# Kernel tuning notes

Hardware: AMD Instinct MI355X
Metric: run time of the kernel (lower is better)

The kernel has to match this reference:

```python
import jax, jax.numpy as jnp
import numpy as np

B, L, D = 4096, 200, 64


def setup_inputs() -> dict:
    key = jax.random.key(0)
    ks = jax.random.split(key, 7)
    target_key = jax.random.normal(ks[0], (B, D), dtype=jnp.float32)
    item_keys = jax.random.normal(ks[1], (B, L, D), dtype=jnp.float32)
    item_values = jax.random.normal(ks[2], (B, L, D), dtype=jnp.float32)
    mask = jax.random.randint(ks[3], (B, L), 0, 2, dtype=jnp.int32)
    # Linear(D, D, bias=False) weights; torch applies y = x @ W.T
    scale = 1.0 / np.sqrt(D)
    W_target = jax.random.uniform(ks[4], (D, D), jnp.float32, -scale, scale)
    W_item = jax.random.uniform(ks[5], (D, D), jnp.float32, -scale, scale)
    W_value = jax.random.uniform(ks[6], (D, D), jnp.float32, -scale, scale)
    return {
        "target_key": target_key,
        "item_keys": item_keys,
        "item_values": item_values,
        "mask": mask,
        "W_target": W_target,
        "W_item": W_item,
        "W_value": W_value,
    }


def reference(target_key, item_keys, item_values, mask, W_target, W_item, W_value):
    scaler = jnp.float32(D) ** 0.5
    q = target_key @ W_target.T                      # [B, D]
    k = jnp.einsum("bld,ed->ble", item_keys, W_item)   # [B, L, D]
    v = jnp.einsum("bld,ed->ble", item_values, W_value) # [B, L, D]
    # single-query scores: broadcast multiply + reduce over D
    scores = jnp.einsum("bd,bld->bl", q, k) / scaler  # [B, L]
    scores = scores + (-1e8) * (1.0 - mask.astype(scores.dtype))
    w = jax.nn.softmax(scores, axis=1)                # softmax over L
    return jnp.einsum("bl,bld->bd", w, v)             # [B, D]
```

## Files before the change

### kernel.cpp

```cpp
#include <hip/hip_runtime.h>


#define B_ 4096
#define L_ 200
#define D_ 64

__global__ __launch_bounds__(256) void ta_kernel(
    const float* __restrict__ tk,
    const float* __restrict__ ik,
    const float* __restrict__ iv,
    const int*   __restrict__ mask,
    const float* __restrict__ Wt,
    const float* __restrict__ Wi,
    const float* __restrict__ Wv,
    float* __restrict__ out)
{
  const int t = threadIdx.x;
  const int b = blockIdx.x;
  const int c  = t & 15;
  const int rg = t >> 4;

  __shared__ float q_s[D_];
  __shared__ float qt_s[D_];
  __shared__ float bias_s[L_];
  __shared__ float sc[L_];
  __shared__ float red[8];
  __shared__ float vred[256 * 4];
  __shared__ float sv[D_];

  if (t < L_) {
    int m = mask[(size_t)b * L_ + t];
    bias_s[t] = m ? 0.0f : -1e8f;
  }

  if (t < D_) {
    const float4* tkb4 = (const float4*)(tk + (size_t)b * D_);
    const float4* Wt4  = (const float4*)Wt;
    float a = 0.f;
#pragma unroll
    for (int j = 0; j < 16; ++j) {
      float4 w = Wt4[t * 16 + j];
      float4 x = tkb4[j];
      a += w.x * x.x + w.y * x.y + w.z * x.z + w.w * x.w;
    }
    q_s[t] = a;
  }
  __syncthreads();
  if (t < D_) {
    float a = 0.f;
#pragma unroll
    for (int e = 0; e < D_; ++e) a += q_s[e] * Wi[e * D_ + t];
    qt_s[t] = a;
  }
  __syncthreads();

  const float4* ik4 = (const float4*)(ik + (size_t)b * (L_ * D_));
  const float4* q4  = (const float4*)qt_s;
  const float4 qc = q4[c];
#pragma unroll
  for (int it = 0; it < 13; ++it) {
    int row = it * 16 + rg;
    float p = 0.f;
    if (row < L_) {
      float4 kv = ik4[it * 256 + t];
      p = kv.x * qc.x + kv.y * qc.y + kv.z * qc.z + kv.w * qc.w;
    }
    p += __shfl_xor(p, 8, 64);
    p += __shfl_xor(p, 4, 64);
    p += __shfl_xor(p, 2, 64);
    p += __shfl_xor(p, 1, 64);
    if (c == 0 && row < L_) sc[row] = p * 0.125f + bias_s[row];
  }
  __syncthreads();

  float v = (t < L_) ? sc[t] : -3.0e38f;
#pragma unroll
  for (int off = 32; off >= 1; off >>= 1)
    v = fmaxf(v, __shfl_xor(v, off, 64));
  if ((t & 63) == 0) red[t >> 6] = v;
  __syncthreads();
  float mx = fmaxf(fmaxf(red[0], red[1]), fmaxf(red[2], red[3]));
  float ex = (t < L_) ? expf(sc[t] - mx) : 0.f;
  float s = ex;
#pragma unroll
  for (int off = 32; off >= 1; off >>= 1)
    s += __shfl_xor(s, off, 64);
  if ((t & 63) == 0) red[4 + (t >> 6)] = s;
  __syncthreads();
  float tot = red[4] + red[5] + red[6] + red[7];
  if (t < L_) sc[t] = ex / tot;
  __syncthreads();

  const float4* iv4 = (const float4*)(iv + (size_t)b * (L_ * D_));
  float4 acc = make_float4(0.f, 0.f, 0.f, 0.f);
#pragma unroll
  for (int it = 0; it < 13; ++it) {
    int row = it * 16 + rg;
    if (row < L_) {
      float w = sc[row];
      float4 vv = iv4[it * 256 + t];
      acc.x += w * vv.x; acc.y += w * vv.y;
      acc.z += w * vv.z; acc.w += w * vv.w;
    }
  }
  ((float4*)vred)[t] = acc;
  __syncthreads();
  if (t < D_) {
    float a = 0.f;
#pragma unroll
    for (int rg2 = 0; rg2 < 16; ++rg2) a += vred[rg2 * 64 + t];
    sv[t] = a;
  }
  __syncthreads();

  if (t < D_) {
    const float4* Wv4 = (const float4*)Wv;
    const float4* sv4 = (const float4*)sv;
    float a = 0.f;
#pragma unroll
    for (int cc = 0; cc < 16; ++cc) {
      float4 w4 = Wv4[t * 16 + cc];
      float4 s4 = sv4[cc];
      a += w4.x * s4.x + w4.y * s4.y + w4.z * s4.z + w4.w * s4.w;
    }
    out[(size_t)b * D_ + t] = a;
  }
}

extern "C" void kernel_launch(void* const* d_in, const int* in_sizes, int n_in,
                              void* d_out, int out_size, void* d_ws, size_t ws_size,
                              hipStream_t stream) {
  const float* tk   = (const float*)d_in[0];
  const float* ik   = (const float*)d_in[1];
  const float* iv   = (const float*)d_in[2];
  const int*   mask = (const int*)  d_in[3];
  const float* Wt   = (const float*)d_in[4];
  const float* Wi   = (const float*)d_in[5];
  const float* Wv   = (const float*)d_in[6];
  float* out = (float*)d_out;

  ta_kernel<<<B_, 256, 0, stream>>>(tk, ik, iv, mask, Wt, Wi, Wv, out);
}
```

Baseline: 431.0 us.

## Prefetch all key and value rows into registers before the softmax phase

Loads each block's full key and value tiles into registers up front, 13 float4 each per thread, so the value reads are issued early and overlap the score and softmax computation instead of waiting until after it. Pads the score array to 208 entries with zeros so the weighted-sum loop needs no bounds checks. Adds a launch-bounds occupancy hint of 3 blocks per CU. The extra 104 registers per thread may cut occupancy or cause spills.

```diff
diff --git a/kernel.cpp b/kernel.cpp
--- a/kernel.cpp
+++ b/kernel.cpp
@@ -5,7 +5,7 @@
 #define L_ 200
 #define D_ 64
 
-__global__ __launch_bounds__(256) void ta_kernel(
+__global__ __launch_bounds__(256, 3) void ta_kernel(
     const float* __restrict__ tk,
     const float* __restrict__ ik,
     const float* __restrict__ iv,
@@ -23,7 +23,7 @@
   __shared__ float q_s[D_];
   __shared__ float qt_s[D_];
   __shared__ float bias_s[L_];
-  __shared__ float sc[L_];
+  __shared__ float sc[208];
   __shared__ float red[8];
   __shared__ float vred[256 * 4];
   __shared__ float sv[D_];
@@ -55,20 +55,25 @@
   __syncthreads();
 
   const float4* ik4 = (const float4*)(ik + (size_t)b * (L_ * D_));
-  const float4* q4  = (const float4*)qt_s;
-  const float4 qc = q4[c];
+  const float4* iv4 = (const float4*)(iv + (size_t)b * (L_ * D_));
+  float4 K[13], V[13];
+#pragma unroll
+  for (int it = 0; it < 12; ++it) K[it] = ik4[it * 256 + t];
+  K[12] = (192 + rg < L_) ? ik4[12 * 256 + t] : make_float4(0.f, 0.f, 0.f, 0.f);
+#pragma unroll
+  for (int it = 0; it < 12; ++it) V[it] = iv4[it * 256 + t];
+  V[12] = (192 + rg < L_) ? iv4[12 * 256 + t] : make_float4(0.f, 0.f, 0.f, 0.f);
+
+  const float4 qc = ((const float4*)qt_s)[c];
 #pragma unroll
   for (int it = 0; it < 13; ++it) {
-    int row = it * 16 + rg;
-    float p = 0.f;
-    if (row < L_) {
-      float4 kv = ik4[it * 256 + t];
-      p = kv.x * qc.x + kv.y * qc.y + kv.z * qc.z + kv.w * qc.w;
-    }
+    float4 kv = K[it];
+    float p = kv.x * qc.x + kv.y * qc.y + kv.z * qc.z + kv.w * qc.w;
     p += __shfl_xor(p, 8, 64);
     p += __shfl_xor(p, 4, 64);
     p += __shfl_xor(p, 2, 64);
     p += __shfl_xor(p, 1, 64);
+    int row = it * 16 + rg;
     if (c == 0 && row < L_) sc[row] = p * 0.125f + bias_s[row];
   }
   __syncthreads();
@@ -88,20 +93,16 @@
   if ((t & 63) == 0) red[4 + (t >> 6)] = s;
   __syncthreads();
   float tot = red[4] + red[5] + red[6] + red[7];
-  if (t < L_) sc[t] = ex / tot;
+  if (t < L_)      sc[t] = ex / tot;
+  else if (t < 208) sc[t] = 0.f;
   __syncthreads();
 
-  const float4* iv4 = (const float4*)(iv + (size_t)b * (L_ * D_));
   float4 acc = make_float4(0.f, 0.f, 0.f, 0.f);
 #pragma unroll
   for (int it = 0; it < 13; ++it) {
-    int row = it * 16 + rg;
-    if (row < L_) {
-      float w = sc[row];
-      float4 vv = iv4[it * 256 + t];
-      acc.x += w * vv.x; acc.y += w * vv.y;
-      acc.z += w * vv.z; acc.w += w * vv.w;
-    }
+    float w = sc[it * 16 + rg];
+    acc.x += w * V[it].x; acc.y += w * V[it].y;
+    acc.z += w * V[it].z; acc.w += w * V[it].w;
   }
   ((float4*)vred)[t] = acc;
   __syncthreads();
```

Measured after the change: 415.6 us. 3.6% less time.
